# Kernel tuning notes

Hardware: AMD Instinct MI355X
Metric: run time of the kernel (lower is better)

The kernel has to match this reference:

```python
import jax, jax.numpy as jnp
import numpy as np

B, S, E = 2, 2048, 2048
H, HKV, KQV = 16, 4, 2048
D = KQV // H            # 128 head dim
KV_DIM = D * HKV        # 512
WINDOW = 256
NEG = jnp.finfo(jnp.float32).min


def setup_inputs() -> dict:
    key = jax.random.key(0)
    ks = jax.random.split(key, 5)
    sc = 0.02
    return {
        "hidden_states": jax.random.normal(ks[0], (B, S, E), jnp.float32),
        "Wq": jax.random.normal(ks[1], (KQV, E), jnp.float32) * sc,
        "Wk": jax.random.normal(ks[2], (KV_DIM, E), jnp.float32) * sc,
        "Wv": jax.random.normal(ks[3], (KV_DIM, E), jnp.float32) * sc,
        "Wo": jax.random.normal(ks[4], (E, KQV), jnp.float32) * sc,
        "bo": jnp.zeros((E,), jnp.float32),
    }


def reference(hidden_states, Wq, Wk, Wv, Wo, bo):
    x = hidden_states
    # projections (nn.Linear: x @ W.T)
    q = (x @ Wq.T).reshape(B, S, H, D).transpose(0, 2, 1, 3)      # [B,H,S,D]
    k = (x @ Wk.T).reshape(B, S, HKV, D).transpose(0, 2, 1, 3)    # [B,HKV,S,D]
    v = (x @ Wv.T).reshape(B, S, HKV, D).transpose(0, 2, 1, 3)

    # faithful reproduction of the module's index_select head expansion:
    # group_sizes are uniform (H % HKV == 0); both query and kv indices are
    # [0]*g + [1]*g + ... so query head i (i < HKV) is duplicated g times.
    idx = jnp.repeat(jnp.arange(HKV), H // HKV)                   # [H]
    qs = q[:, idx]                                                # [B,H,S,D]
    ks = k[:, idx]
    vs = v[:, idx]

    # GPT-Neo style: no 1/sqrt(D) scaling
    scores = jnp.einsum('bhqd,bhkd->bhqk', qs, ks)                # [B,H,S,S]

    i = jnp.arange(S)[:, None]
    j = jnp.arange(S)[None, :]
    # local causal mask: j <= i and j > i - WINDOW
    mask = (j <= i) & (j > i - WINDOW)                            # [S,S]
    scores = jnp.where(mask[None, None], scores, NEG)
    attn = jax.nn.softmax(scores, axis=-1)

    out = jnp.einsum('bhqk,bhkd->bhqd', attn, vs)                 # [B,H,S,D]
    out = out.transpose(0, 2, 1, 3).reshape(B, S, H * D)          # merge heads
    return out @ Wo.T + bo
```

## Files before the change

### kernel.cpp

```cpp
#include <hip/hip_runtime.h>

typedef _Float16 f16;
typedef _Float16 f16x8 __attribute__((ext_vector_type(8)));
typedef _Float16 f16x4 __attribute__((ext_vector_type(4)));
typedef float    f32x4 __attribute__((ext_vector_type(4)));


__device__ __forceinline__ void load_lds16(const void* g, void* l) {
    __builtin_amdgcn_global_load_lds(
        (__attribute__((address_space(1))) void*)(g),
        (__attribute__((address_space(3))) void*)(l), 16, 0, 0);
}

__global__ __launch_bounds__(256)
void cvt_pack(const float* __restrict__ X, const float* __restrict__ Wq,
              const float* __restrict__ Wk, const float* __restrict__ Wv,
              const float* __restrict__ Wo,
              f16* __restrict__ Xp, f16* __restrict__ Wp, f16* __restrict__ Wrp)
{
    const int blk = blockIdx.x, tid = threadIdx.x;
    if (blk < 4096) {
        int cid = blk * 256 + tid;
        int tile = cid >> 8, wc = cid & 255;
        int row = wc >> 2, kc = wc & 3;
        int m = ((tile >> 6) << 6) + row;
        int t = tile & 63;
        int sk = t * 32 + ((kc ^ ((row >> 1) & 3)) << 3);
        const float* s = X + (size_t)m * 2048 + sk;
        float4 a = *(const float4*)(s);
        float4 b = *(const float4*)(s + 4);
        f16x8 o;
        o[0]=(f16)a.x; o[1]=(f16)a.y; o[2]=(f16)a.z; o[3]=(f16)a.w;
        o[4]=(f16)b.x; o[5]=(f16)b.y; o[6]=(f16)b.z; o[7]=(f16)b.w;
        *(f16x8*)(Xp + (size_t)cid * 8) = o;
    } else if (blk < 5632) {
        int wid = (blk - 4096) * 256 + tid;
        int tile = wid >> 9, wc = wid & 511;
        int row = wc >> 2, kc = wc & 3;
        int n = ((tile >> 6) << 7) + row;
        int t = tile & 63;
        int sk = t * 32 + ((kc ^ ((row >> 1) & 3)) << 3);
        const float* src = (n < 512)  ? (Wq + (size_t)n * 2048 + sk)
                         : (n < 1024) ? (Wk + (size_t)(n - 512) * 2048 + sk)
                                      : (Wv + (size_t)(n - 1024) * 2048 + sk);
        float4 a = *(const float4*)(src);
        float4 b = *(const float4*)(src + 4);
        f16x8 o;
        o[0]=(f16)a.x; o[1]=(f16)a.y; o[2]=(f16)a.z; o[3]=(f16)a.w;
        o[4]=(f16)b.x; o[5]=(f16)b.y; o[6]=(f16)b.z; o[7]=(f16)b.w;
        *(f16x8*)(Wp + (size_t)wid * 8) = o;
    } else {
        int rid = (blk - 5632) * 256 + tid;
        int tile = rid >> 9, wc = rid & 511;
        int row = wc >> 2, kc = wc & 3;
        int e = ((tile >> 4) << 7) + row;
        int t = tile & 15;
        int cc = kc ^ ((row >> 1) & 3);
        int c = t * 32 + (cc << 3);
        int g = c >> 7, d0 = c & 127;
        const float* src = Wo + (size_t)e * 2048 + g * 512 + d0;
        float4 a0 = *(const float4*)(src);
        float4 a1 = *(const float4*)(src + 128);
        float4 a2 = *(const float4*)(src + 256);
        float4 a3 = *(const float4*)(src + 384);
        float4 b0 = *(const float4*)(src + 4);
        float4 b1 = *(const float4*)(src + 132);
        float4 b2 = *(const float4*)(src + 260);
        float4 b3 = *(const float4*)(src + 388);
        f16x8 o;
        o[0] = (f16)(a0.x + a1.x + a2.x + a3.x);
        o[1] = (f16)(a0.y + a1.y + a2.y + a3.y);
        o[2] = (f16)(a0.z + a1.z + a2.z + a3.z);
        o[3] = (f16)(a0.w + a1.w + a2.w + a3.w);
        o[4] = (f16)(b0.x + b1.x + b2.x + b3.x);
        o[5] = (f16)(b0.y + b1.y + b2.y + b3.y);
        o[6] = (f16)(b0.z + b1.z + b2.z + b3.z);
        o[7] = (f16)(b0.w + b1.w + b2.w + b3.w);
        *(f16x8*)(Wrp + (size_t)rid * 8) = o;
    }
}

__global__ __launch_bounds__(256)
void qkv_gemm(const f16* __restrict__ Xp, const f16* __restrict__ Wp,
              f16* __restrict__ Qo, f16* __restrict__ Ko, f16* __restrict__ Vo)
{
    const int NSTEP = 64;
    __shared__ __align__(16) f16 S[4][8192];

    const int tid = threadIdx.x;
    const int wave = tid >> 6, lane = tid & 63;
    const int lrow = lane & 15, lquad = lane >> 4;
    const int wr = wave >> 1, wc = wave & 1;

    int id = (int)blockIdx.x;
    int id2 = (id & 7) * 48 + (id >> 3);
    int bx = id2 % 12, by = id2 / 12;
    const int m0 = by * 128;

    const f16* gA0 = Xp + (size_t)(2 * by)     * 131072 + (size_t)tid * 8;
    const f16* gA1 = Xp + (size_t)(2 * by + 1) * 131072 + (size_t)tid * 8;
    const f16* gB0 = Wp + (size_t)bx * 262144 + (size_t)tid * 8;
    const f16* gB1 = Wp + (size_t)bx * 262144 + (size_t)(256 + tid) * 8;
    const int loA0 = tid * 8;
    const int loA1 = (256 + tid) * 8;
    const int loB0 = (512 + tid) * 8;
    const int loB1 = (768 + tid) * 8;

#define QSTAGE(t, buf)                                             \
    {                                                              \
        load_lds16(gA0 + (size_t)(t) * 2048, &S[buf][loA0]);       \
        load_lds16(gA1 + (size_t)(t) * 2048, &S[buf][loA1]);       \
        load_lds16(gB0 + (size_t)(t) * 4096, &S[buf][loB0]);       \
        load_lds16(gB1 + (size_t)(t) * 4096, &S[buf][loB1]);       \
    }

    int aoff[4], boff[4];
#pragma unroll
    for (int t = 0; t < 4; t++) {
        int ra = wr * 64 + t * 16 + lrow;
        aoff[t] = ra * 32 + ((lquad ^ ((ra >> 1) & 3)) << 3);
        int rb = wc * 64 + t * 16 + lrow;
        boff[t] = 4096 + rb * 32 + ((lquad ^ ((rb >> 1) & 3)) << 3);
    }

    f32x4 acc[4][4];
    const f32x4 z4 = {0.f, 0.f, 0.f, 0.f};
#pragma unroll
    for (int i = 0; i < 4; i++) for (int j = 0; j < 4; j++) acc[i][j] = z4;

    QSTAGE(0, 0); QSTAGE(1, 1); QSTAGE(2, 2);

    int buf = 0;
    for (int t = 0; t < NSTEP; ++t) {
        if (t < NSTEP - 2) {
            asm volatile("s_waitcnt vmcnt(8) lgkmcnt(0)" ::: "memory");
        } else if (t == NSTEP - 2) {
            asm volatile("s_waitcnt vmcnt(4) lgkmcnt(0)" ::: "memory");
        } else {
            asm volatile("s_waitcnt vmcnt(0) lgkmcnt(0)" ::: "memory");
        }
        __builtin_amdgcn_s_barrier();
        if (t < NSTEP - 3) QSTAGE(t + 3, (buf + 3) & 3);
        f16x8 af[4], bf[4];
#pragma unroll
        for (int mt = 0; mt < 4; mt++) af[mt] = *(const f16x8*)(&S[buf][aoff[mt]]);
#pragma unroll
        for (int nt = 0; nt < 4; nt++) bf[nt] = *(const f16x8*)(&S[buf][boff[nt]]);
#pragma unroll
        for (int mt = 0; mt < 4; mt++)
#pragma unroll
            for (int nt = 0; nt < 4; nt++)
                acc[mt][nt] = __builtin_amdgcn_mfma_f32_16x16x32_f16(af[mt], bf[nt], acc[mt][nt], 0, 0, 0);
        buf = (buf + 1) & 3;
    }
#undef QSTAGE

    const int z = bx >> 2;
    const int hh = bx & 3;
    if (z == 0) {
#pragma unroll
        for (int mt = 0; mt < 4; mt++) {
            int mbase = m0 + wr * 64 + mt * 16 + lquad * 4;
#pragma unroll
            for (int r = 0; r < 4; r++) {
                int m = mbase + r;
                int bb = m >> 11, s = m & 2047;
#pragma unroll
                for (int nt = 0; nt < 4; nt++) {
                    int d = wc * 64 + nt * 16 + lrow;
                    Qo[(size_t)(((bb * 4 + hh) << 11) + s) * 128 + d] = (f16)acc[mt][nt][r];
                }
            }
        }
    } else if (z == 1) {
#pragma unroll
        for (int mt = 0; mt < 4; mt++) {
            int mbase = m0 + wr * 64 + mt * 16 + lquad * 4;
#pragma unroll
            for (int r = 0; r < 4; r++) {
                int m = mbase + r;
                int bb = m >> 11, s = m & 2047;
                size_t base = ((size_t)(bb * 4 + hh) * 16 + (s >> 7)) * 16384
                            + (size_t)(s & 127) * 128;
#pragma unroll
                for (int nt = 0; nt < 4; nt++) {
                    int d = wc * 64 + nt * 16 + lrow;
                    Ko[base + (((d >> 3) ^ (s & 15)) << 3) + (d & 7)] = (f16)acc[mt][nt][r];
                }
            }
        }
    } else {
#pragma unroll
        for (int mt = 0; mt < 4; mt++) {
            int mbase = m0 + wr * 64 + mt * 16 + lquad * 4;
            int bb = mbase >> 11, s = mbase & 2047;
            int tt = s >> 6, sl = s & 63;
            int gsx = sl >> 3, j0 = sl & 7;
#pragma unroll
            for (int nt = 0; nt < 4; nt++) {
                int d = wc * 64 + nt * 16 + lrow;
                f16x4 pk;
#pragma unroll
                for (int r = 0; r < 4; r++) pk[r] = (f16)acc[mt][nt][r];
                *(f16x4*)(Vo + ((size_t)(bb * 4 + hh) * 32 + tt) * 8192
                             + (size_t)d * 64 + ((gsx ^ (d & 7)) << 3) + j0) = pk;
            }
        }
    }
}

__global__ __launch_bounds__(512, 2)
void attn_win(const f16* __restrict__ Q, const f16* __restrict__ Kp,
              const f16* __restrict__ Vp, f16* __restrict__ AO)
{
    const int hblk = blockIdx.x;
    const int bg = hblk & 7, qt = hblk >> 3;
    const int b = bg >> 2, g = bg & 3;
    const int qbase = qt * 64;
    const int tid = threadIdx.x;
    const int wave = tid >> 6, lane = tid & 63;
    const int lrow = lane & 15, lquad = lane >> 4;
    const int qg = wave >> 1, hf = wave & 1;
    const int qw = qbase + qg * 16;

    const f16* Qb = Q  + (size_t)bg * (2048 * 128);
    const f16* Kt = Kp + (size_t)bg * 262144;
    const f16* Vt = Vp + (size_t)bg * 262144;

    __shared__ __align__(16) f16 Ks[2][2][8192];
    __shared__ __align__(16) f16 Vs[2][2][8192];
    __shared__ __align__(16) f16 Pl[8][1024];

    f16x8 qf[4];
#pragma unroll
    for (int ks = 0; ks < 4; ks++)
        qf[ks] = *(const f16x8*)(Qb + (size_t)(qw + lrow) * 128 + ks * 32 + lquad * 8);

    float m_i[4], l_i[4];
    f32x4 oa[8];
    const f32x4 z4 = {0.f, 0.f, 0.f, 0.f};
#pragma unroll
    for (int r = 0; r < 4; r++) { m_i[r] = -30000.f; l_i[r] = 0.f; }
#pragma unroll
    for (int nt = 0; nt < 8; nt++) oa[nt] = z4;

    const int t0v = (qbase >= 256) ? ((qbase - 255) >> 6) : 0;
    const int t1v = (qbase + 63) >> 6;
    const int T = t1v - t0v + 1;
    const int I = (T + 1) >> 1;

    const int c0 = (wave * 64 + lane) * 8;
    const int c1 = c0 + 4096;

#define APAIR(p, bufi)                                                         \
    {                                                                          \
        int tA = t0v + 2 * (p);  if (tA > t1v) tA = t1v;                       \
        int tB = tA + 1;         if (tB > t1v) tB = t1v;                       \
        const f16* kA = Kt + (size_t)(tA >> 1) * 16384 + (size_t)(tA & 1) * 8192; \
        const f16* vA = Vt + (size_t)tA * 8192;                                \
        const f16* kB = Kt + (size_t)(tB >> 1) * 16384 + (size_t)(tB & 1) * 8192; \
        const f16* vB = Vt + (size_t)tB * 8192;                                \
        load_lds16(kA + c0, &Ks[0][bufi][c0]);                                 \
        load_lds16(kA + c1, &Ks[0][bufi][c1]);                                 \
        load_lds16(vA + c0, &Vs[0][bufi][c0]);                                 \
        load_lds16(vA + c1, &Vs[0][bufi][c1]);                                 \
        load_lds16(kB + c0, &Ks[1][bufi][c0]);                                 \
        load_lds16(kB + c1, &Ks[1][bufi][c1]);                                 \
        load_lds16(vB + c0, &Vs[1][bufi][c0]);                                 \
        load_lds16(vB + c1, &Vs[1][bufi][c1]);                                 \
    }

    APAIR(0, 0);
    APAIR(1, 1);

    int bufc = 0;
    for (int i = 0; i < I; ++i) {
        if (i < I - 1) asm volatile("s_waitcnt vmcnt(8)" ::: "memory");
        else           asm volatile("s_waitcnt vmcnt(0)" ::: "memory");
        __builtin_amdgcn_s_barrier();

        const int t = t0v + 2 * i + hf;
        if (t <= t1v) {
            const int kt = t * 64;
            f32x4 sc[4];
#pragma unroll
            for (int nt = 0; nt < 4; nt++) sc[nt] = z4;
#pragma unroll
            for (int nt = 0; nt < 4; nt++) {
#pragma unroll
                for (int ks = 0; ks < 4; ks++) {
                    f16x8 kf = *(const f16x8*)(&Ks[hf][bufc][(nt * 16 + lrow) * 128
                                      + (((ks * 4 + lquad) ^ lrow) << 3)]);
                    sc[nt] = __builtin_amdgcn_mfma_f32_16x16x32_f16(qf[ks], kf, sc[nt], 0, 0, 0);
                }
            }
#pragma unroll
            for (int r = 0; r < 4; r++) {
                const int qi = qw + lquad * 4 + r;
                float rmax = -60000.f;
#pragma unroll
                for (int nt = 0; nt < 4; nt++) {
                    int kj = kt + nt * 16 + lrow;
                    float sval = sc[nt][r];
                    bool ok = (kj <= qi) && (kj + 256 > qi);
                    sval = ok ? sval : -60000.f;
                    sc[nt][r] = sval;
                    rmax = fmaxf(rmax, sval);
                }
                rmax = fmaxf(rmax, __shfl_xor(rmax, 1));
                rmax = fmaxf(rmax, __shfl_xor(rmax, 2));
                rmax = fmaxf(rmax, __shfl_xor(rmax, 4));
                rmax = fmaxf(rmax, __shfl_xor(rmax, 8));
                float mold = m_i[r];
                float mnew = fmaxf(mold, rmax);
                float alpha = __expf(mold - mnew);
                m_i[r] = mnew;
                float rsum = 0.f;
#pragma unroll
                for (int nt = 0; nt < 4; nt++) {
                    float p = __expf(sc[nt][r] - mnew);
                    sc[nt][r] = p;
                    rsum += p;
                }
                rsum += __shfl_xor(rsum, 1);
                rsum += __shfl_xor(rsum, 2);
                rsum += __shfl_xor(rsum, 4);
                rsum += __shfl_xor(rsum, 8);
                l_i[r] = l_i[r] * alpha + rsum;
#pragma unroll
                for (int nt = 0; nt < 8; nt++) oa[nt][r] *= alpha;
            }
#pragma unroll
            for (int nt = 0; nt < 4; nt++)
#pragma unroll
                for (int r = 0; r < 4; r++) {
                    int row = lquad * 4 + r;
                    Pl[wave][row * 64 + (((nt * 2 + (lrow >> 3)) ^ (row & 7)) << 3)
                             + (lrow & 7)] = (f16)sc[nt][r];
                }
            f16x8 pf[2];
#pragma unroll
            for (int ks = 0; ks < 2; ks++)
                pf[ks] = *(const f16x8*)(&Pl[wave][lrow * 64
                                  + (((ks * 4 + lquad) ^ (lrow & 7)) << 3)]);
#pragma unroll
            for (int nt = 0; nt < 8; nt++) {
#pragma unroll
                for (int ks = 0; ks < 2; ks++) {
                    int dv = nt * 16 + lrow;
                    f16x8 vf = *(const f16x8*)(&Vs[hf][bufc][dv * 64
                                      + (((ks * 4 + lquad) ^ (dv & 7)) << 3)]);
                    oa[nt] = __builtin_amdgcn_mfma_f32_16x16x32_f16(pf[ks], vf, oa[nt], 0, 0, 0);
                }
            }
        }
        asm volatile("s_waitcnt lgkmcnt(0)" ::: "memory");
        __builtin_amdgcn_s_barrier();
        if (i + 2 < I) APAIR(i + 2, bufc);
        bufc ^= 1;
    }
#undef APAIR

    float* mrg = (float*)&Ks[0][0][0];
    if (hf == 1) {
#pragma unroll
        for (int r = 0; r < 4; r++) {
            int row = lquad * 4 + r;
            if (lrow == 0) {
                mrg[qg * 16 + row] = m_i[r];
                mrg[64 + qg * 16 + row] = l_i[r];
            }
#pragma unroll
            for (int nt = 0; nt < 8; nt++)
                mrg[128 + qg * 2048 + row * 128 + nt * 16 + lrow] = oa[nt][r];
        }
    }
    asm volatile("s_waitcnt lgkmcnt(0)" ::: "memory");
    __builtin_amdgcn_s_barrier();
    if (hf == 0) {
#pragma unroll
        for (int r = 0; r < 4; r++) {
            int row = lquad * 4 + r;
            float m1 = mrg[qg * 16 + row];
            float l1 = mrg[64 + qg * 16 + row];
            float mm = fmaxf(m_i[r], m1);
            float a0 = __expf(m_i[r] - mm);
            float a1 = __expf(m1 - mm);
            float ll = l_i[r] * a0 + l1 * a1;
            float inv = (ll > 0.f) ? 1.f / ll : 0.f;
            int q = qw + row;
            int m = b * 2048 + q;
            int p = m >> 6, r2 = m & 63;
#pragma unroll
            for (int nt = 0; nt < 8; nt++) {
                int d = nt * 16 + lrow;
                float o1 = mrg[128 + qg * 2048 + row * 128 + d];
                float od = (oa[nt][r] * a0 + o1 * a1) * inv;
                int col = g * 128 + d;
                int tt = col >> 5;
                int cc = (col >> 3) & 3;
                size_t off = (((size_t)p * 16 + tt) * 64 + r2) * 32
                           + ((cc ^ ((r2 >> 1) & 3)) << 3) + (col & 7);
                AO[off] = (f16)od;
            }
        }
    }
}

__global__ __launch_bounds__(256)
void out_gemm(const f16* __restrict__ Ap, const f16* __restrict__ Bp,
              const float* __restrict__ bias, float* __restrict__ C)
{
    const int NSTEP = 16, N = 2048;
    __shared__ __align__(16) f16 S[4][8192];

    const int tid = threadIdx.x;
    const int wave = tid >> 6, lane = tid & 63;
    const int lrow = lane & 15, lquad = lane >> 4;
    const int wr = wave >> 1, wc = wave & 1;

    int id = (int)blockIdx.x;
    int id2 = (id & 7) * 64 + (id >> 3);
    int bx = id2 & 15, by = id2 >> 4;
    const int m0 = by * 128, n0 = bx * 128;

    const f16* gA0 = Ap + (size_t)(2 * by)     * 32768 + (size_t)tid * 8;
    const f16* gA1 = Ap + (size_t)(2 * by + 1) * 32768 + (size_t)tid * 8;
    const f16* gB0 = Bp + (size_t)bx * 65536 + (size_t)tid * 8;
    const f16* gB1 = Bp + (size_t)bx * 65536 + (size_t)(256 + tid) * 8;
    const int loA0 = tid * 8;
    const int loA1 = (256 + tid) * 8;
    const int loB0 = (512 + tid) * 8;
    const int loB1 = (768 + tid) * 8;

#define OSTAGE(t, buf)                                             \
    {                                                              \
        load_lds16(gA0 + (size_t)(t) * 2048, &S[buf][loA0]);       \
        load_lds16(gA1 + (size_t)(t) * 2048, &S[buf][loA1]);       \
        load_lds16(gB0 + (size_t)(t) * 4096, &S[buf][loB0]);       \
        load_lds16(gB1 + (size_t)(t) * 4096, &S[buf][loB1]);       \
    }

    int aoff[4], boff[4];
#pragma unroll
    for (int t = 0; t < 4; t++) {
        int ra = wr * 64 + t * 16 + lrow;
        aoff[t] = ra * 32 + ((lquad ^ ((ra >> 1) & 3)) << 3);
        int rb = wc * 64 + t * 16 + lrow;
        boff[t] = 4096 + rb * 32 + ((lquad ^ ((rb >> 1) & 3)) << 3);
    }

    f32x4 acc[4][4];
    const f32x4 z4 = {0.f, 0.f, 0.f, 0.f};
#pragma unroll
    for (int i = 0; i < 4; i++) for (int j = 0; j < 4; j++) acc[i][j] = z4;

    OSTAGE(0, 0); OSTAGE(1, 1); OSTAGE(2, 2);

    int buf = 0;
    for (int t = 0; t < NSTEP; ++t) {
        if (t < NSTEP - 2) {
            asm volatile("s_waitcnt vmcnt(8) lgkmcnt(0)" ::: "memory");
        } else if (t == NSTEP - 2) {
            asm volatile("s_waitcnt vmcnt(4) lgkmcnt(0)" ::: "memory");
        } else {
            asm volatile("s_waitcnt vmcnt(0) lgkmcnt(0)" ::: "memory");
        }
        __builtin_amdgcn_s_barrier();
        if (t < NSTEP - 3) OSTAGE(t + 3, (buf + 3) & 3);
        f16x8 af[4], bf[4];
#pragma unroll
        for (int mt = 0; mt < 4; mt++) af[mt] = *(const f16x8*)(&S[buf][aoff[mt]]);
#pragma unroll
        for (int nt = 0; nt < 4; nt++) bf[nt] = *(const f16x8*)(&S[buf][boff[nt]]);
#pragma unroll
        for (int mt = 0; mt < 4; mt++)
#pragma unroll
            for (int nt = 0; nt < 4; nt++)
                acc[mt][nt] = __builtin_amdgcn_mfma_f32_16x16x32_f16(af[mt], bf[nt], acc[mt][nt], 0, 0, 0);
        buf = (buf + 1) & 3;
    }

#pragma unroll
    for (int nt = 0; nt < 4; nt++) {
        int n = n0 + wc * 64 + nt * 16 + lrow;
        float bv2 = bias[n];
#pragma unroll
        for (int mt = 0; mt < 4; mt++) {
            int mbase = m0 + wr * 64 + mt * 16 + lquad * 4;
#pragma unroll
            for (int r = 0; r < 4; r++)
                C[(size_t)(mbase + r) * N + n] = acc[mt][nt][r] + bv2;
        }
    }
#undef OSTAGE
}

extern "C" void kernel_launch(void* const* d_in, const int* in_sizes, int n_in,
                              void* d_out, int out_size, void* d_ws, size_t ws_size,
                              hipStream_t stream)
{
    const float* x  = (const float*)d_in[0];
    const float* Wq = (const float*)d_in[1];
    const float* Wk = (const float*)d_in[2];
    const float* Wv = (const float*)d_in[3];
    const float* Wo = (const float*)d_in[4];
    const float* bo = (const float*)d_in[5];
    float* out = (float*)d_out;

    f16* Xp  = (f16*)d_ws;
    f16* AO  = Xp;
    f16* Wp  = Xp  + 8388608;
    f16* Wrp = Wp  + 3145728;
    f16* Qws = Wrp + 1048576;
    f16* Kws = Qws + 2097152;
    f16* Vws = Kws + 2097152;

    cvt_pack<<<dim3(6144), 256, 0, stream>>>(x, Wq, Wk, Wv, Wo, Xp, Wp, Wrp);
    qkv_gemm<<<dim3(384), 256, 0, stream>>>(Xp, Wp, Qws, Kws, Vws);
    attn_win<<<dim3(256), 512, 0, stream>>>(Qws, Kws, Vws, AO);
    out_gemm<<<dim3(512), 256, 0, stream>>>(AO, Wrp, bo, out);
}
```

Before: 175.1 us.

## Widen QKV GEMM tile to 128x192 so 256 blocks cover the grid

The QKV projection GEMM tile grows from 128x128 to 128x192 output columns, and the grid shrinks from 384 to 256 blocks, one per CU on a 256-CU part. This removes the partial second wave of blocks and raises MFMA work per LDS load. Load staging is regenerated for 5 chunks per thread, the waitcnt thresholds are adjusted, and the epilogue picks the Q/K/V destination per column tile. The cost is more accumulator registers (24 f32x4 tiles), a larger LDS footprint, and removal of the previous block-swizzle ordering.

```diff
diff --git a/kernel.cpp b/kernel.cpp
--- a/kernel.cpp
+++ b/kernel.cpp
@@ -85,120 +85,123 @@
               f16* __restrict__ Qo, f16* __restrict__ Ko, f16* __restrict__ Vo)
 {
     const int NSTEP = 64;
-    __shared__ __align__(16) f16 S[4][8192];
+    __shared__ __align__(16) f16 S[4][10240];
 
     const int tid = threadIdx.x;
     const int wave = tid >> 6, lane = tid & 63;
     const int lrow = lane & 15, lquad = lane >> 4;
     const int wr = wave >> 1, wc = wave & 1;
 
-    int id = (int)blockIdx.x;
-    int id2 = (id & 7) * 48 + (id >> 3);
-    int bx = id2 % 12, by = id2 / 12;
+    const int id = (int)blockIdx.x;
+    const int bx = id & 7;
+    const int by = id >> 3;
     const int m0 = by * 128;
 
-    const f16* gA0 = Xp + (size_t)(2 * by)     * 131072 + (size_t)tid * 8;
-    const f16* gA1 = Xp + (size_t)(2 * by + 1) * 131072 + (size_t)tid * 8;
-    const f16* gB0 = Wp + (size_t)bx * 262144 + (size_t)tid * 8;
-    const f16* gB1 = Wp + (size_t)bx * 262144 + (size_t)(256 + tid) * 8;
-    const int loA0 = tid * 8;
-    const int loA1 = (256 + tid) * 8;
-    const int loB0 = (512 + tid) * 8;
-    const int loB1 = (768 + tid) * 8;
-
-#define QSTAGE(t, buf)                                             \
-    {                                                              \
-        load_lds16(gA0 + (size_t)(t) * 2048, &S[buf][loA0]);       \
-        load_lds16(gA1 + (size_t)(t) * 2048, &S[buf][loA1]);       \
-        load_lds16(gB0 + (size_t)(t) * 4096, &S[buf][loB0]);       \
-        load_lds16(gB1 + (size_t)(t) * 4096, &S[buf][loB1]);       \
-    }
-
-    int aoff[4], boff[4];
+    const f16* gs[5]; int st[5]; int lo[5];
+#pragma unroll
+    for (int j = 0; j < 5; j++) {
+        int c = (wave * 5 + j) * 64 + lane;
+        lo[j] = c * 8;
+        if (c < 512) {
+            gs[j] = Xp + (size_t)(2 * by + (c >> 8)) * 131072 + (size_t)(c & 255) * 8;
+            st[j] = 2048;
+        } else {
+            int cb = c - 512;
+            int rb = cb >> 2, kc = cb & 3;
+            int n = bx * 192 + rb;
+            gs[j] = Wp + (size_t)(n >> 7) * 262144 + (size_t)((n & 127) * 32 + kc * 8);
+            st[j] = 4096;
+        }
+    }
+
+#define QSTAGE(t, buf)                                                  \
+    {                                                                   \
+        _Pragma("unroll")                                               \
+        for (int j = 0; j < 5; j++)                                     \
+            load_lds16(gs[j] + (size_t)(t) * st[j], &S[buf][lo[j]]);    \
+    }
+
+    int aoff[4], boff[6];
 #pragma unroll
     for (int t = 0; t < 4; t++) {
         int ra = wr * 64 + t * 16 + lrow;
         aoff[t] = ra * 32 + ((lquad ^ ((ra >> 1) & 3)) << 3);
-        int rb = wc * 64 + t * 16 + lrow;
+    }
+#pragma unroll
+    for (int t = 0; t < 6; t++) {
+        int rb = wc * 96 + t * 16 + lrow;
         boff[t] = 4096 + rb * 32 + ((lquad ^ ((rb >> 1) & 3)) << 3);
     }
 
-    f32x4 acc[4][4];
+    f32x4 acc[4][6];
     const f32x4 z4 = {0.f, 0.f, 0.f, 0.f};
 #pragma unroll
-    for (int i = 0; i < 4; i++) for (int j = 0; j < 4; j++) acc[i][j] = z4;
+    for (int i = 0; i < 4; i++) for (int j = 0; j < 6; j++) acc[i][j] = z4;
 
     QSTAGE(0, 0); QSTAGE(1, 1); QSTAGE(2, 2);
 
     int buf = 0;
     for (int t = 0; t < NSTEP; ++t) {
         if (t < NSTEP - 2) {
-            asm volatile("s_waitcnt vmcnt(8) lgkmcnt(0)" ::: "memory");
+            asm volatile("s_waitcnt vmcnt(10) lgkmcnt(0)" ::: "memory");
         } else if (t == NSTEP - 2) {
-            asm volatile("s_waitcnt vmcnt(4) lgkmcnt(0)" ::: "memory");
+            asm volatile("s_waitcnt vmcnt(5) lgkmcnt(0)" ::: "memory");
         } else {
             asm volatile("s_waitcnt vmcnt(0) lgkmcnt(0)" ::: "memory");
         }
         __builtin_amdgcn_s_barrier();
         if (t < NSTEP - 3) QSTAGE(t + 3, (buf + 3) & 3);
-        f16x8 af[4], bf[4];
+        f16x8 af[4], bf[6];
 #pragma unroll
         for (int mt = 0; mt < 4; mt++) af[mt] = *(const f16x8*)(&S[buf][aoff[mt]]);
 #pragma unroll
-        for (int nt = 0; nt < 4; nt++) bf[nt] = *(const f16x8*)(&S[buf][boff[nt]]);
+        for (int nt = 0; nt < 6; nt++) bf[nt] = *(const f16x8*)(&S[buf][boff[nt]]);
 #pragma unroll
         for (int mt = 0; mt < 4; mt++)
 #pragma unroll
-            for (int nt = 0; nt < 4; nt++)
+            for (int nt = 0; nt < 6; nt++)
                 acc[mt][nt] = __builtin_amdgcn_mfma_f32_16x16x32_f16(af[mt], bf[nt], acc[mt][nt], 0, 0, 0);
         buf = (buf + 1) & 3;
     }
 #undef QSTAGE
 
-    const int z = bx >> 2;
-    const int hh = bx & 3;
-    if (z == 0) {
-#pragma unroll
-        for (int mt = 0; mt < 4; mt++) {
-            int mbase = m0 + wr * 64 + mt * 16 + lquad * 4;
-#pragma unroll
-            for (int r = 0; r < 4; r++) {
-                int m = mbase + r;
-                int bb = m >> 11, s = m & 2047;
-#pragma unroll
-                for (int nt = 0; nt < 4; nt++) {
-                    int d = wc * 64 + nt * 16 + lrow;
+#pragma unroll
+    for (int nt = 0; nt < 6; nt++) {
+        const int n = bx * 192 + wc * 96 + nt * 16 + lrow;
+        const int z = n >> 9;
+        const int hh = (n >> 7) & 3;
+        const int d = n & 127;
+        if (z == 0) {
+#pragma unroll
+            for (int mt = 0; mt < 4; mt++) {
+                int mbase = m0 + wr * 64 + mt * 16 + lquad * 4;
+#pragma unroll
+                for (int r = 0; r < 4; r++) {
+                    int m = mbase + r;
+                    int bb = m >> 11, s = m & 2047;
                     Qo[(size_t)(((bb * 4 + hh) << 11) + s) * 128 + d] = (f16)acc[mt][nt][r];
                 }
             }
-        }
-    } else if (z == 1) {
-#pragma unroll
-        for (int mt = 0; mt < 4; mt++) {
-            int mbase = m0 + wr * 64 + mt * 16 + lquad * 4;
-#pragma unroll
-            for (int r = 0; r < 4; r++) {
-                int m = mbase + r;
-                int bb = m >> 11, s = m & 2047;
-                size_t base = ((size_t)(bb * 4 + hh) * 16 + (s >> 7)) * 16384
-                            + (size_t)(s & 127) * 128;
-#pragma unroll
-                for (int nt = 0; nt < 4; nt++) {
-                    int d = wc * 64 + nt * 16 + lrow;
+        } else if (z == 1) {
+#pragma unroll
+            for (int mt = 0; mt < 4; mt++) {
+                int mbase = m0 + wr * 64 + mt * 16 + lquad * 4;
+#pragma unroll
+                for (int r = 0; r < 4; r++) {
+                    int m = mbase + r;
+                    int bb = m >> 11, s = m & 2047;
+                    size_t base = ((size_t)(bb * 4 + hh) * 16 + (s >> 7)) * 16384
+                                + (size_t)(s & 127) * 128;
                     Ko[base + (((d >> 3) ^ (s & 15)) << 3) + (d & 7)] = (f16)acc[mt][nt][r];
                 }
             }
-        }
-    } else {
-#pragma unroll
-        for (int mt = 0; mt < 4; mt++) {
-            int mbase = m0 + wr * 64 + mt * 16 + lquad * 4;
-            int bb = mbase >> 11, s = mbase & 2047;
-            int tt = s >> 6, sl = s & 63;
-            int gsx = sl >> 3, j0 = sl & 7;
-#pragma unroll
-            for (int nt = 0; nt < 4; nt++) {
-                int d = wc * 64 + nt * 16 + lrow;
+        } else {
+#pragma unroll
+            for (int mt = 0; mt < 4; mt++) {
+                int mbase = m0 + wr * 64 + mt * 16 + lquad * 4;
+                int bb = mbase >> 11, s = mbase & 2047;
+                int tt = s >> 6, sl = s & 63;
+                int gsx = sl >> 3, j0 = sl & 7;
                 f16x4 pk;
 #pragma unroll
                 for (int r = 0; r < 4; r++) pk[r] = (f16)acc[mt][nt][r];
@@ -517,7 +520,7 @@
     f16* Vws = Kws + 2097152;
 
     cvt_pack<<<dim3(6144), 256, 0, stream>>>(x, Wq, Wk, Wv, Wo, Xp, Wp, Wrp);
-    qkv_gemm<<<dim3(384), 256, 0, stream>>>(Xp, Wp, Qws, Kws, Vws);
+    qkv_gemm<<<dim3(256), 256, 0, stream>>>(Xp, Wp, Qws, Kws, Vws);
     attn_win<<<dim3(256), 512, 0, stream>>>(Qws, Kws, Vws, AO);
     out_gemm<<<dim3(512), 256, 0, stream>>>(AO, Wrp, bo, out);
 }
```

New measurement: 174.2 us. Within noise of the previous version (-0.5%).
